# Optimization experiments

Hardware: AMD Instinct MI355X
Metric: run time of the kernel (lower is better)

The kernel has to match this reference:

```python
import jax, jax.numpy as jnp
import numpy as np

B = 128
N = 512            # num_nodes
RU = 64            # rnn_units = hidden_size // num_nodes
IN_PER_NODE = 2    # input_size // num_nodes
MEM_DIM = 16
BOT_DIM = 4
IN_SZ = IN_PER_NODE + RU      # 66, concat(input, state) per node
OUT_SZ = 4 * RU               # 256, 4 LSTM gates


def setup_inputs() -> dict:
    key = jax.random.key(0)
    ks = jax.random.split(key, 12)
    std = 1.0 / np.sqrt(N * RU)  # reset_parameters: uniform(-std, std)
    u = lambda k, shape: jax.random.uniform(k, shape, jnp.float32, -std, std)
    return {
        "inputs": jax.random.normal(ks[0], (B, N * IN_PER_NODE), jnp.float32),
        "hx": jax.random.normal(ks[1], (B, N * RU), jnp.float32),
        "cx": jax.random.normal(ks[2], (B, N * RU), jnp.float32),
        "memory": u(ks[3], (N, MEM_DIM)),
        "w1": u(ks[4], (MEM_DIM, MEM_DIM)),
        "b1": u(ks[5], (MEM_DIM,)),
        "w2": u(ks[6], (MEM_DIM, BOT_DIM)),
        "b2": u(ks[7], (BOT_DIM,)),
        "w3": u(ks[8], (BOT_DIM, IN_SZ * OUT_SZ)),
        "b3": u(ks[9], (IN_SZ * OUT_SZ,)),
        "b_out": u(ks[10], (OUT_SZ,)),
    }


def reference(inputs, hx, cx, memory, w1, b1, w2, b2, w3, b3, b_out):
    b = inputs.shape[0]
    n = memory.shape[0]
    ru = hx.shape[1] // n
    # per-node concat of input and state: [B, N, IN_SZ]
    x = inputs.reshape(b, n, -1)
    h = hx.reshape(b, n, ru)
    xs = jnp.concatenate([x, h], axis=-1)
    # hypernetwork: memory -> per-node weight matrices [N, IN_SZ, OUT_SZ]
    mem = jnp.tanh(memory @ w1 + b1)
    mem = jnp.tanh(mem @ w2 + b2)
    W = (mem @ w3 + b3).reshape(n, xs.shape[-1], -1)
    # batched per-node matmul (original repeats W over batch; same math without the repeat)
    val = jax.nn.sigmoid(jnp.einsum('bni,nio->bno', xs, W)) + b_out  # [B, N, 4*RU]
    g = val.reshape(b, n, 4, ru)
    i_t = jax.nn.sigmoid(g[:, :, 0, :].reshape(b, n * ru))
    f_t = jax.nn.sigmoid(g[:, :, 1, :].reshape(b, n * ru))
    g_t = jnp.tanh(g[:, :, 2, :].reshape(b, n * ru))
    o_t = jax.nn.sigmoid(g[:, :, 3, :].reshape(b, n * ru))
    cy = cx * f_t + i_t * g_t
    hy = o_t * jnp.tanh(cy)
    return hy, cy
```

## Files before the change

### kernel.cpp

```cpp
#include <hip/hip_runtime.h>
#include <math.h>

#define BATCH 128
#define NNODE 512
#define RU 64
#define MEM_DIM 16
#define BOT_DIM 4
#define IN_SZ 66
#define OUT_SZ 256
#define HID (NNODE*RU)
#define W3_ROW 16896
#define COL_SHORTS 104
#define NODE_W_SHORTS (256*COL_SHORTS)
#define HALF_W_SHORTS (128*COL_SHORTS)

typedef __attribute__((ext_vector_type(8))) short short8;
typedef __attribute__((ext_vector_type(4))) float float4v;

__device__ __forceinline__ unsigned short f2bf(float f) {
    unsigned int u = __float_as_uint(f);
    unsigned int r = (u + 0x7FFFu + ((u >> 16) & 1u)) >> 16;
    return (unsigned short)r;
}
__device__ __forceinline__ float fsig(float x) {
    return __builtin_amdgcn_rcpf(1.0f + __expf(-x));
}
__device__ __forceinline__ float ftanh(float x) {
    return 1.0f - 2.0f * __builtin_amdgcn_rcpf(1.0f + __expf(2.0f * x));
}

__global__ __launch_bounds__(256) void wgen_kernel(
    const float* __restrict__ memory, const float* __restrict__ w1,
    const float* __restrict__ b1,     const float* __restrict__ w2,
    const float* __restrict__ b2,     const float* __restrict__ w3,
    const float* __restrict__ b3,     unsigned short* __restrict__ W_ws)
{
    __shared__ unsigned short Wn[256][COL_SHORTS];
    const int c = threadIdx.x;
    const int n = blockIdx.x;

    float memv[MEM_DIM];
    #pragma unroll
    for (int j = 0; j < MEM_DIM; ++j) memv[j] = memory[n * MEM_DIM + j];
    float mem1[MEM_DIM];
    #pragma unroll
    for (int t = 0; t < MEM_DIM; ++t) {
        float s = b1[t];
        #pragma unroll
        for (int j = 0; j < MEM_DIM; ++j) s += memv[j] * w1[j * MEM_DIM + t];
        mem1[t] = ftanh(s);
    }
    float m[BOT_DIM];
    #pragma unroll
    for (int t = 0; t < BOT_DIM; ++t) {
        float s = b2[t];
        #pragma unroll
        for (int j = 0; j < MEM_DIM; ++j) s += mem1[j] * w2[j * BOT_DIM + t];
        m[t] = ftanh(s);
    }

    const int ct = c >> 4, q = c & 15;
    const int o = (ct & 3) * 64 + (ct >> 2) * 16 + q;
    const float* p0 = w3 + o;
    const float* pb = b3 + o;

    for (int i = 0; i < IN_SZ; ++i) {
        int j = i * OUT_SZ;
        float f = pb[j] + m[0] * p0[j] + m[1] * p0[W3_ROW + j]
                        + m[2] * p0[2 * W3_ROW + j] + m[3] * p0[3 * W3_ROW + j];
        int s = (i < 2) ? (64 + i) : (i - 2);
        Wn[c][s] = f2bf(f);
    }
    #pragma unroll
    for (int s = IN_SZ; s < COL_SHORTS; ++s) Wn[c][s] = 0;
    __syncthreads();

    unsigned short* dst = W_ws + (size_t)n * NODE_W_SHORTS + c * COL_SHORTS;
    #pragma unroll
    for (int kc = 0; kc < 13; ++kc)
        *(short8*)(dst + kc * 8) = *(const short8*)(&Wn[c][kc * 8]);
}

__global__ __launch_bounds__(256, 3) void gemm_kernel(
    const float* __restrict__ inputs, const float* __restrict__ hx,
    const float* __restrict__ cx,     const float* __restrict__ b_out,
    const unsigned short* __restrict__ W_ws, float* __restrict__ out)
{
    __shared__ unsigned short Wl[128][COL_SHORTS];
    const int tid  = threadIdx.x;
    const int n    = (int)blockIdx.x >> 1;
    const int h    = (int)blockIdx.x & 1;
    const int w    = tid >> 6;
    const int lane = tid & 63;
    const int q    = lane & 15;
    const int quad = lane >> 4;

    const unsigned short* gW = W_ws + (size_t)n * NODE_W_SHORTS + h * HALF_W_SHORTS;
    for (int t = w; t < 26; t += 4) {
        __builtin_amdgcn_global_load_lds(
            (__attribute__((address_space(1))) void*)(gW + t * 512 + lane * 8),
            (__attribute__((address_space(3))) void*)(&Wl[0][0] + t * 512),
            16, 0, 0);
    }

    short8 a[3][2];
    #pragma unroll
    for (int rt = 0; rt < 2; ++rt) {
        const int row = w * 32 + rt * 16 + q;
        const float* hrow = hx + (size_t)row * HID + n * RU + quad * 8;
        #pragma unroll
        for (int ks = 0; ks < 2; ++ks) {
            float4v f0 = *(const float4v*)(hrow + ks * 32);
            float4v f1 = *(const float4v*)(hrow + ks * 32 + 4);
            short8 t;
            t[0] = (short)f2bf(f0[0]); t[1] = (short)f2bf(f0[1]);
            t[2] = (short)f2bf(f0[2]); t[3] = (short)f2bf(f0[3]);
            t[4] = (short)f2bf(f1[0]); t[5] = (short)f2bf(f1[1]);
            t[6] = (short)f2bf(f1[2]); t[7] = (short)f2bf(f1[3]);
            a[ks][rt] = t;
        }
        short8 t2 = {0, 0, 0, 0, 0, 0, 0, 0};
        if (quad == 0) {
            const float* ip = inputs + (size_t)row * (NNODE * IN_SZ - NNODE * RU) + n * 2;
            t2[0] = (short)f2bf(ip[0]);
            t2[1] = (short)f2bf(ip[1]);
        }
        a[2][rt] = t2;
    }

    float4v acc[2][8];
    #pragma unroll
    for (int rt = 0; rt < 2; ++rt)
        #pragma unroll
        for (int ctl = 0; ctl < 8; ++ctl)
            acc[rt][ctl] = (float4v){0.f, 0.f, 0.f, 0.f};

    __syncthreads();

    #pragma unroll
    for (int ks = 0; ks < 3; ++ks) {
        #pragma unroll
        for (int ctl = 0; ctl < 8; ++ctl) {
            short8 bfrag = *(const short8*)(&Wl[ctl * 16 + q][(ks * 4 + quad) * 8]);
            acc[0][ctl] = __builtin_amdgcn_mfma_f32_16x16x32_bf16(a[ks][0], bfrag, acc[0][ctl], 0, 0, 0);
            acc[1][ctl] = __builtin_amdgcn_mfma_f32_16x16x32_bf16(a[ks][1], bfrag, acc[1][ctl], 0, 0, 0);
        }
    }

    float bo[2][4];
    #pragma unroll
    for (int rh = 0; rh < 2; ++rh)
        #pragma unroll
        for (int g = 0; g < 4; ++g)
            bo[rh][g] = b_out[g * 64 + (h * 2 + rh) * 16 + q];

    #pragma unroll
    for (int rt = 0; rt < 2; ++rt) {
        #pragma unroll
        for (int v = 0; v < 4; ++v) {
            const int b = w * 32 + rt * 16 + quad * 4 + v;
            const size_t base = (size_t)b * HID + n * RU;
            #pragma unroll
            for (int rh = 0; rh < 2; ++rh) {
                float vi = fsig(acc[rt][rh * 4 + 0][v]) + bo[rh][0];
                float vf = fsig(acc[rt][rh * 4 + 1][v]) + bo[rh][1];
                float vg = fsig(acc[rt][rh * 4 + 2][v]) + bo[rh][2];
                float vo = fsig(acc[rt][rh * 4 + 3][v]) + bo[rh][3];
                float it = fsig(vi), ft = fsig(vf);
                float gt = ftanh(vg), ot = fsig(vo);
                const size_t idx = base + (h * 2 + rh) * 16 + q;
                float cc = cx[idx] * ft + it * gt;
                out[idx] = ot * ftanh(cc);
                out[(size_t)BATCH * HID + idx] = cc;
            }
        }
    }
}

extern "C" void kernel_launch(void* const* d_in, const int* in_sizes, int n_in,
                              void* d_out, int out_size, void* d_ws, size_t ws_size,
                              hipStream_t stream) {
    const float* inputs = (const float*)d_in[0];
    const float* hx     = (const float*)d_in[1];
    const float* cx     = (const float*)d_in[2];
    const float* memory = (const float*)d_in[3];
    const float* w1     = (const float*)d_in[4];
    const float* b1     = (const float*)d_in[5];
    const float* w2     = (const float*)d_in[6];
    const float* b2     = (const float*)d_in[7];
    const float* w3     = (const float*)d_in[8];
    const float* b3     = (const float*)d_in[9];
    const float* b_out  = (const float*)d_in[10];
    float* out = (float*)d_out;

    unsigned short* W_ws = (unsigned short*)d_ws;

    wgen_kernel<<<NNODE, 256, 0, stream>>>(memory, w1, b1, w2, b2, w3, b3, W_ws);
    gemm_kernel<<<NNODE * 2, 256, 0, stream>>>(inputs, hx, cx, b_out, W_ws, out);
}
```

Measured before the change: 139.4 us.

## Tile weight-generation by output-column groups and prefetch cx before MFMA loop

The weight-generation kernel now stages a 32-column slice of w3 and b3 in shared memory once per block and reuses it across 8 nodes. Previously every node block re-read all of w3 and b3 from global memory. The output is written as coalesced 16-byte chunks. The GEMM kernel loads cx and b_out into registers before the MFMA loop so those loads overlap the matrix work, at the cost of extra registers under launch bounds of 3 blocks per SM.

```diff
diff --git a/kernel.cpp b/kernel.cpp
--- a/kernel.cpp
+++ b/kernel.cpp
@@ -13,6 +13,8 @@
 #define COL_SHORTS 104
 #define NODE_W_SHORTS (256*COL_SHORTS)
 #define HALF_W_SHORTS (128*COL_SHORTS)
+#define W3S_STRIDE 84
+#define B3S_STRIDE 72
 
 typedef __attribute__((ext_vector_type(8))) short short8;
 typedef __attribute__((ext_vector_type(4))) float float4v;
@@ -27,6 +29,10 @@
 }
 __device__ __forceinline__ float ftanh(float x) {
     return 1.0f - 2.0f * __builtin_amdgcn_rcpf(1.0f + __expf(2.0f * x));
+}
+__device__ __forceinline__ int omap(int cg, int cl) {
+    int ct = cg * 2 + (cl >> 4);
+    return (ct & 3) * 64 + ((ct >> 2) << 4) + (cl & 15);
 }
 
 __global__ __launch_bounds__(256) void wgen_kernel(
@@ -35,50 +41,92 @@
     const float* __restrict__ b2,     const float* __restrict__ w3,
     const float* __restrict__ b3,     unsigned short* __restrict__ W_ws)
 {
-    __shared__ unsigned short Wn[256][COL_SHORTS];
-    const int c = threadIdx.x;
-    const int n = blockIdx.x;
-
-    float memv[MEM_DIM];
-    #pragma unroll
-    for (int j = 0; j < MEM_DIM; ++j) memv[j] = memory[n * MEM_DIM + j];
-    float mem1[MEM_DIM];
-    #pragma unroll
-    for (int t = 0; t < MEM_DIM; ++t) {
+    __shared__ alignas(16) float w3s[4][32][W3S_STRIDE];
+    __shared__ alignas(16) float b3s[32][B3S_STRIDE];
+    __shared__ float mem1s[8][MEM_DIM];
+    __shared__ float m2s[8][BOT_DIM];
+
+    const int tid = threadIdx.x;
+    const int cg  = (int)blockIdx.x & 7;
+    const int ng  = (int)blockIdx.x >> 3;
+
+    for (int e = tid; e < 4 * 32 * 72; e += 256) {
+        int cl = e & 31;
+        int r  = e >> 5;
+        int k  = r / 72;
+        int s  = r - k * 72;
+        float v = 0.f;
+        if (s < 66) {
+            int i = (s < 64) ? s + 2 : s - 64;
+            v = w3[k * W3_ROW + i * OUT_SZ + omap(cg, cl)];
+        }
+        w3s[k][cl][s] = v;
+    }
+    for (int e = tid; e < 32 * 72; e += 256) {
+        int cl = e & 31;
+        int s  = e >> 5;
+        float v = 0.f;
+        if (s < 66) {
+            int i = (s < 64) ? s + 2 : s - 64;
+            v = b3[i * OUT_SZ + omap(cg, cl)];
+        }
+        b3s[cl][s] = v;
+    }
+
+    if (tid < 128) {
+        int nn = tid >> 4, t = tid & 15;
+        int n  = ng * 8 + nn;
         float s = b1[t];
         #pragma unroll
-        for (int j = 0; j < MEM_DIM; ++j) s += memv[j] * w1[j * MEM_DIM + t];
-        mem1[t] = ftanh(s);
-    }
-    float m[BOT_DIM];
-    #pragma unroll
-    for (int t = 0; t < BOT_DIM; ++t) {
+        for (int j = 0; j < MEM_DIM; ++j)
+            s += memory[n * MEM_DIM + j] * w1[j * MEM_DIM + t];
+        mem1s[nn][t] = ftanh(s);
+    }
+    __syncthreads();
+    if (tid < 32) {
+        int nn = tid >> 2, t = tid & 3;
         float s = b2[t];
         #pragma unroll
-        for (int j = 0; j < MEM_DIM; ++j) s += mem1[j] * w2[j * BOT_DIM + t];
-        m[t] = ftanh(s);
-    }
-
-    const int ct = c >> 4, q = c & 15;
-    const int o = (ct & 3) * 64 + (ct >> 2) * 16 + q;
-    const float* p0 = w3 + o;
-    const float* pb = b3 + o;
-
-    for (int i = 0; i < IN_SZ; ++i) {
-        int j = i * OUT_SZ;
-        float f = pb[j] + m[0] * p0[j] + m[1] * p0[W3_ROW + j]
-                        + m[2] * p0[2 * W3_ROW + j] + m[3] * p0[3 * W3_ROW + j];
-        int s = (i < 2) ? (64 + i) : (i - 2);
-        Wn[c][s] = f2bf(f);
-    }
-    #pragma unroll
-    for (int s = IN_SZ; s < COL_SHORTS; ++s) Wn[c][s] = 0;
+        for (int j = 0; j < MEM_DIM; ++j)
+            s += mem1s[nn][j] * w2[j * BOT_DIM + t];
+        m2s[nn][t] = ftanh(s);
+    }
     __syncthreads();
 
-    unsigned short* dst = W_ws + (size_t)n * NODE_W_SHORTS + c * COL_SHORTS;
-    #pragma unroll
-    for (int kc = 0; kc < 13; ++kc)
-        *(short8*)(dst + kc * 8) = *(const short8*)(&Wn[c][kc * 8]);
+    for (int p = 0; p < 4; ++p) {
+        const int n0 = ng * 8 + p * 2;
+        float ma[4], mb[4];
+        #pragma unroll
+        for (int k = 0; k < 4; ++k) { ma[k] = m2s[p * 2][k]; mb[k] = m2s[p * 2 + 1][k]; }
+
+        for (int t = tid; t < 832; t += 256) {
+            int nn2 = t >= 416;
+            int rem = nn2 ? t - 416 : t;
+            int cl  = rem / 13;
+            int sc  = rem - cl * 13;
+            short8 ov = {0, 0, 0, 0, 0, 0, 0, 0};
+            if (sc < 9) {
+                const int s0 = sc * 8;
+                float4v v0 = *(const float4v*)&b3s[cl][s0];
+                float4v v1 = *(const float4v*)&b3s[cl][s0 + 4];
+                #pragma unroll
+                for (int k = 0; k < 4; ++k) {
+                    float mk = nn2 ? mb[k] : ma[k];
+                    float4v w0 = *(const float4v*)&w3s[k][cl][s0];
+                    float4v w1v = *(const float4v*)&w3s[k][cl][s0 + 4];
+                    v0 += mk * w0;
+                    v1 += mk * w1v;
+                }
+                ov[0] = (short)f2bf(v0[0]); ov[1] = (short)f2bf(v0[1]);
+                ov[2] = (short)f2bf(v0[2]); ov[3] = (short)f2bf(v0[3]);
+                ov[4] = (short)f2bf(v1[0]); ov[5] = (short)f2bf(v1[1]);
+                ov[6] = (short)f2bf(v1[2]); ov[7] = (short)f2bf(v1[3]);
+            }
+            unsigned short* dst = W_ws + (size_t)(n0 + nn2) * NODE_W_SHORTS
+                                + cg * 3328 + cl * COL_SHORTS + sc * 8;
+            *(short8*)dst = ov;
+        }
+    }
 }
 
 __global__ __launch_bounds__(256, 3) void gemm_kernel(
@@ -121,12 +169,30 @@
         }
         short8 t2 = {0, 0, 0, 0, 0, 0, 0, 0};
         if (quad == 0) {
-            const float* ip = inputs + (size_t)row * (NNODE * IN_SZ - NNODE * RU) + n * 2;
+            const float* ip = inputs + (size_t)row * (NNODE * 2) + n * 2;
             t2[0] = (short)f2bf(ip[0]);
             t2[1] = (short)f2bf(ip[1]);
         }
         a[2][rt] = t2;
     }
+
+    float cxr[2][4][2];
+    #pragma unroll
+    for (int rt = 0; rt < 2; ++rt)
+        #pragma unroll
+        for (int v = 0; v < 4; ++v) {
+            const int b = w * 32 + rt * 16 + quad * 4 + v;
+            #pragma unroll
+            for (int rh = 0; rh < 2; ++rh)
+                cxr[rt][v][rh] = cx[(size_t)b * HID + n * RU + (h * 2 + rh) * 16 + q];
+        }
+
+    float bo[2][4];
+    #pragma unroll
+    for (int rh = 0; rh < 2; ++rh)
+        #pragma unroll
+        for (int g = 0; g < 4; ++g)
+            bo[rh][g] = b_out[g * 64 + (h * 2 + rh) * 16 + q];
 
     float4v acc[2][8];
     #pragma unroll
@@ -146,13 +212,6 @@
             acc[1][ctl] = __builtin_amdgcn_mfma_f32_16x16x32_bf16(a[ks][1], bfrag, acc[1][ctl], 0, 0, 0);
         }
     }
-
-    float bo[2][4];
-    #pragma unroll
-    for (int rh = 0; rh < 2; ++rh)
-        #pragma unroll
-        for (int g = 0; g < 4; ++g)
-            bo[rh][g] = b_out[g * 64 + (h * 2 + rh) * 16 + q];
 
     #pragma unroll
     for (int rt = 0; rt < 2; ++rt) {
@@ -169,7 +228,7 @@
                 float it = fsig(vi), ft = fsig(vf);
                 float gt = ftanh(vg), ot = fsig(vo);
                 const size_t idx = base + (h * 2 + rh) * 16 + q;
-                float cc = cx[idx] * ft + it * gt;
+                float cc = cxr[rt][v][rh] * ft + it * gt;
                 out[idx] = ot * ftanh(cc);
                 out[(size_t)BATCH * HID + idx] = cc;
             }
```

Result: no change. 136.7 us (-1.9%).

## Pre-swizzle weights into MFMA fragment order and split GEMM into quarter-node blocks

Applied to the files above, without the earlier changes.

The weight generator now writes bf16 weights directly in per-lane MFMA B-fragment order, and each block handles two nodes so every w3/b3 load is reused twice. The GEMM kernel drops the LDS staging and the barrier and reads fragments straight from global memory with 16-byte loads. Each block now covers a quarter of a node's output columns, giving 2048 blocks and fewer accumulators, with occupancy raised to 4. cx is prefetched before the MFMA loop. The trade-offs are redundant hx loads across four blocks per node and extra wgen grid work.

```diff
diff --git a/kernel.cpp b/kernel.cpp
--- a/kernel.cpp
+++ b/kernel.cpp
@@ -10,9 +10,8 @@
 #define OUT_SZ 256
 #define HID (NNODE*RU)
 #define W3_ROW 16896
-#define COL_SHORTS 104
-#define NODE_W_SHORTS (256*COL_SHORTS)
-#define HALF_W_SHORTS (128*COL_SHORTS)
+#define NODE_WS 24576
+#define HALF_WS 12288
 
 typedef __attribute__((ext_vector_type(8))) short short8;
 typedef __attribute__((ext_vector_type(4))) float float4v;
@@ -35,73 +34,94 @@
     const float* __restrict__ b2,     const float* __restrict__ w3,
     const float* __restrict__ b3,     unsigned short* __restrict__ W_ws)
 {
-    __shared__ unsigned short Wn[256][COL_SHORTS];
-    const int c = threadIdx.x;
-    const int n = blockIdx.x;
-
-    float memv[MEM_DIM];
-    #pragma unroll
-    for (int j = 0; j < MEM_DIM; ++j) memv[j] = memory[n * MEM_DIM + j];
-    float mem1[MEM_DIM];
-    #pragma unroll
-    for (int t = 0; t < MEM_DIM; ++t) {
+    __shared__ float mem1s[2][MEM_DIM];
+    __shared__ float m2s[2][BOT_DIM];
+
+    const int tid   = threadIdx.x;
+    const unsigned bid = blockIdx.x;
+    const int npair = bid >> 2;
+    const int h     = (bid >> 1) & 1;
+    const int fg    = bid & 1;
+    const int n0    = npair * 2;
+
+    if (tid < 32) {
+        int nn = tid >> 4, t = tid & 15;
         float s = b1[t];
         #pragma unroll
-        for (int j = 0; j < MEM_DIM; ++j) s += memv[j] * w1[j * MEM_DIM + t];
-        mem1[t] = ftanh(s);
-    }
-    float m[BOT_DIM];
-    #pragma unroll
-    for (int t = 0; t < BOT_DIM; ++t) {
+        for (int j = 0; j < MEM_DIM; ++j)
+            s += memory[(n0 + nn) * MEM_DIM + j] * w1[j * MEM_DIM + t];
+        mem1s[nn][t] = ftanh(s);
+    }
+    __syncthreads();
+    if (tid < 8) {
+        int nn = tid >> 2, t = tid & 3;
         float s = b2[t];
         #pragma unroll
-        for (int j = 0; j < MEM_DIM; ++j) s += mem1[j] * w2[j * BOT_DIM + t];
-        m[t] = ftanh(s);
-    }
-
-    const int ct = c >> 4, q = c & 15;
-    const int o = (ct & 3) * 64 + (ct >> 2) * 16 + q;
-    const float* p0 = w3 + o;
-    const float* pb = b3 + o;
-
-    for (int i = 0; i < IN_SZ; ++i) {
-        int j = i * OUT_SZ;
-        float f = pb[j] + m[0] * p0[j] + m[1] * p0[W3_ROW + j]
-                        + m[2] * p0[2 * W3_ROW + j] + m[3] * p0[3 * W3_ROW + j];
-        int s = (i < 2) ? (64 + i) : (i - 2);
-        Wn[c][s] = f2bf(f);
-    }
-    #pragma unroll
-    for (int s = IN_SZ; s < COL_SHORTS; ++s) Wn[c][s] = 0;
+        for (int j = 0; j < MEM_DIM; ++j)
+            s += mem1s[nn][j] * w2[j * BOT_DIM + t];
+        m2s[nn][t] = ftanh(s);
+    }
     __syncthreads();
 
-    unsigned short* dst = W_ws + (size_t)n * NODE_W_SHORTS + c * COL_SHORTS;
-    #pragma unroll
-    for (int kc = 0; kc < 13; ++kc)
-        *(short8*)(dst + kc * 8) = *(const short8*)(&Wn[c][kc * 8]);
-}
-
-__global__ __launch_bounds__(256, 3) void gemm_kernel(
+    float ma[4], mb[4];
+    #pragma unroll
+    for (int k = 0; k < 4; ++k) { ma[k] = m2s[0][k]; mb[k] = m2s[1][k]; }
+
+    unsigned short* dst0 = W_ws + (size_t)n0 * NODE_WS + h * HALF_WS;
+    unsigned short* dst1 = dst0 + NODE_WS;
+
+    #pragma unroll 2
+    for (int it = 0; it < 6; ++it) {
+        const int cid = it * 256 + tid;
+        const int fl  = fg * 12 + (cid >> 6);
+        const int l   = cid & 63;
+        const int ctl = fl / 3;
+        const int ks  = fl - ctl * 3;
+        const int q = l & 15, quad = l >> 4;
+        const int ct = h * 8 + ctl;
+        const int o  = (ct & 3) * 64 + ((ct >> 2) << 4) + q;
+
+        short8 va, vb;
+        #pragma unroll
+        for (int j = 0; j < 8; ++j) {
+            const int s = ks * 32 + quad * 8 + j;
+            float r0 = 0.f, r1 = 0.f;
+            if (s < IN_SZ) {
+                const int i = (s < 64) ? s + 2 : s - 64;
+                const int base = i * OUT_SZ + o;
+                float bb = b3[base];
+                float x0 = w3[base];
+                float x1 = w3[W3_ROW + base];
+                float x2 = w3[2 * W3_ROW + base];
+                float x3 = w3[3 * W3_ROW + base];
+                r0 = bb + ma[0] * x0 + ma[1] * x1 + ma[2] * x2 + ma[3] * x3;
+                r1 = bb + mb[0] * x0 + mb[1] * x1 + mb[2] * x2 + mb[3] * x3;
+            }
+            va[j] = (short)f2bf(r0);
+            vb[j] = (short)f2bf(r1);
+        }
+        const int off = fl * 512 + l * 8;
+        *(short8*)(dst0 + off) = va;
+        *(short8*)(dst1 + off) = vb;
+    }
+}
+
+__global__ __launch_bounds__(256, 4) void gemm_kernel(
     const float* __restrict__ inputs, const float* __restrict__ hx,
     const float* __restrict__ cx,     const float* __restrict__ b_out,
     const unsigned short* __restrict__ W_ws, float* __restrict__ out)
 {
-    __shared__ unsigned short Wl[128][COL_SHORTS];
     const int tid  = threadIdx.x;
-    const int n    = (int)blockIdx.x >> 1;
-    const int h    = (int)blockIdx.x & 1;
+    const unsigned bid = blockIdx.x;
+    const int n    = bid >> 2;
+    const int qh   = bid & 3;
     const int w    = tid >> 6;
     const int lane = tid & 63;
     const int q    = lane & 15;
     const int quad = lane >> 4;
 
-    const unsigned short* gW = W_ws + (size_t)n * NODE_W_SHORTS + h * HALF_W_SHORTS;
-    for (int t = w; t < 26; t += 4) {
-        __builtin_amdgcn_global_load_lds(
-            (__attribute__((address_space(1))) void*)(gW + t * 512 + lane * 8),
-            (__attribute__((address_space(3))) void*)(&Wl[0][0] + t * 512),
-            16, 0, 0);
-    }
+    const unsigned short* Wb = W_ws + (size_t)n * NODE_WS + (qh >> 1) * HALF_WS
+                             + (qh & 1) * 4 * 3 * 512;
 
     short8 a[3][2];
     #pragma unroll
@@ -121,58 +141,59 @@
         }
         short8 t2 = {0, 0, 0, 0, 0, 0, 0, 0};
         if (quad == 0) {
-            const float* ip = inputs + (size_t)row * (NNODE * IN_SZ - NNODE * RU) + n * 2;
+            const float* ip = inputs + (size_t)row * (NNODE * 2) + n * 2;
             t2[0] = (short)f2bf(ip[0]);
             t2[1] = (short)f2bf(ip[1]);
         }
         a[2][rt] = t2;
     }
 
-    float4v acc[2][8];
+    const int r = qh * 16 + q;
+    float bo[4];
+    #pragma unroll
+    for (int g = 0; g < 4; ++g) bo[g] = b_out[g * 64 + r];
+
+    float cxr[2][4];
     #pragma unroll
     for (int rt = 0; rt < 2; ++rt)
-        #pragma unroll
-        for (int ctl = 0; ctl < 8; ++ctl)
-            acc[rt][ctl] = (float4v){0.f, 0.f, 0.f, 0.f};
-
-    __syncthreads();
-
-    #pragma unroll
-    for (int ks = 0; ks < 3; ++ks) {
-        #pragma unroll
-        for (int ctl = 0; ctl < 8; ++ctl) {
-            short8 bfrag = *(const short8*)(&Wl[ctl * 16 + q][(ks * 4 + quad) * 8]);
-            acc[0][ctl] = __builtin_amdgcn_mfma_f32_16x16x32_bf16(a[ks][0], bfrag, acc[0][ctl], 0, 0, 0);
-            acc[1][ctl] = __builtin_amdgcn_mfma_f32_16x16x32_bf16(a[ks][1], bfrag, acc[1][ctl], 0, 0, 0);
-        }
-    }
-
-    float bo[2][4];
-    #pragma unroll
-    for (int rh = 0; rh < 2; ++rh)
-        #pragma unroll
-        for (int g = 0; g < 4; ++g)
-            bo[rh][g] = b_out[g * 64 + (h * 2 + rh) * 16 + q];
-
-    #pragma unroll
-    for (int rt = 0; rt < 2; ++rt) {
         #pragma unroll
         for (int v = 0; v < 4; ++v) {
             const int b = w * 32 + rt * 16 + quad * 4 + v;
-            const size_t base = (size_t)b * HID + n * RU;
-            #pragma unroll
-            for (int rh = 0; rh < 2; ++rh) {
-                float vi = fsig(acc[rt][rh * 4 + 0][v]) + bo[rh][0];
-                float vf = fsig(acc[rt][rh * 4 + 1][v]) + bo[rh][1];
-                float vg = fsig(acc[rt][rh * 4 + 2][v]) + bo[rh][2];
-                float vo = fsig(acc[rt][rh * 4 + 3][v]) + bo[rh][3];
-                float it = fsig(vi), ft = fsig(vf);
-                float gt = ftanh(vg), ot = fsig(vo);
-                const size_t idx = base + (h * 2 + rh) * 16 + q;
-                float cc = cx[idx] * ft + it * gt;
-                out[idx] = ot * ftanh(cc);
-                out[(size_t)BATCH * HID + idx] = cc;
-            }
+            cxr[rt][v] = cx[(size_t)b * HID + n * RU + r];
+        }
+
+    float4v acc[2][4];
+    #pragma unroll
+    for (int rt = 0; rt < 2; ++rt)
+        #pragma unroll
+        for (int g = 0; g < 4; ++g)
+            acc[rt][g] = (float4v){0.f, 0.f, 0.f, 0.f};
+
+    #pragma unroll
+    for (int ks = 0; ks < 3; ++ks) {
+        #pragma unroll
+        for (int g = 0; g < 4; ++g) {
+            short8 bf = *(const short8*)(Wb + (g * 3 + ks) * 512 + lane * 8);
+            acc[0][g] = __builtin_amdgcn_mfma_f32_16x16x32_bf16(a[ks][0], bf, acc[0][g], 0, 0, 0);
+            acc[1][g] = __builtin_amdgcn_mfma_f32_16x16x32_bf16(a[ks][1], bf, acc[1][g], 0, 0, 0);
+        }
+    }
+
+    #pragma unroll
+    for (int rt = 0; rt < 2; ++rt) {
+        #pragma unroll
+        for (int v = 0; v < 4; ++v) {
+            const int b = w * 32 + rt * 16 + quad * 4 + v;
+            const size_t idx = (size_t)b * HID + n * RU + r;
+            float vi = fsig(acc[rt][0][v]) + bo[0];
+            float vf = fsig(acc[rt][1][v]) + bo[1];
+            float vg = fsig(acc[rt][2][v]) + bo[2];
+            float vo = fsig(acc[rt][3][v]) + bo[3];
+            float it = fsig(vi), ft = fsig(vf);
+            float gt = ftanh(vg), ot = fsig(vo);
+            float cc = cxr[rt][v] * ft + it * gt;
+            out[idx] = ot * ftanh(cc);
+            out[(size_t)BATCH * HID + idx] = cc;
         }
     }
 }
@@ -195,6 +216,6 @@
 
     unsigned short* W_ws = (unsigned short*)d_ws;
 
-    wgen_kernel<<<NNODE, 256, 0, stream>>>(memory, w1, b1, w2, b2, w3, b3, W_ws);
-    gemm_kernel<<<NNODE * 2, 256, 0, stream>>>(inputs, hx, cx, b_out, W_ws, out);
-}
+    wgen_kernel<<<256 * 4, 256, 0, stream>>>(memory, w1, b1, w2, b2, w3, b3, W_ws);
+    gemm_kernel<<<NNODE * 4, 256, 0, stream>>>(inputs, hx, cx, b_out, W_ws, out);
+}
```

After: 144.5 us. 1.04x slower.

## Factor hypernetwork weights through rank-5 basis instead of materializing per-node weights

Applied to the files above, without the earlier changes.

Per-node weight matrices W_n = sum_k m_k*w3_k + b3 are no longer built. The kernel instead precomputes five shared bf16 basis matrices (w3 rows and b3) in MFMA fragment layout and scales the activations by each node's coefficient m_k, accumulating five GEMMs. This removes the 512 per-node weight tiles (about 27 MB of workspace written and read back) in exchange for five times the MFMA work and extra bf16 conversions. The basis is small and is read straight from global/L2 without LDS staging. Each node now uses one 512-thread block, and cx is loaded before the matmul.

```diff
diff --git a/kernel.cpp b/kernel.cpp
--- a/kernel.cpp
+++ b/kernel.cpp
@@ -10,9 +10,7 @@
 #define OUT_SZ 256
 #define HID (NNODE*RU)
 #define W3_ROW 16896
-#define COL_SHORTS 104
-#define NODE_W_SHORTS (256*COL_SHORTS)
-#define HALF_W_SHORTS (128*COL_SHORTS)
+#define W5_BYTES (240*512*2)
 
 typedef __attribute__((ext_vector_type(8))) short short8;
 typedef __attribute__((ext_vector_type(4))) float float4v;
@@ -29,150 +27,176 @@
     return 1.0f - 2.0f * __builtin_amdgcn_rcpf(1.0f + __expf(2.0f * x));
 }
 
-__global__ __launch_bounds__(256) void wgen_kernel(
+__global__ __launch_bounds__(256) void prep_kernel(
     const float* __restrict__ memory, const float* __restrict__ w1,
     const float* __restrict__ b1,     const float* __restrict__ w2,
     const float* __restrict__ b2,     const float* __restrict__ w3,
-    const float* __restrict__ b3,     unsigned short* __restrict__ W_ws)
+    const float* __restrict__ b3,     unsigned short* __restrict__ W5,
+    float* __restrict__ m2_ws)
 {
-    __shared__ unsigned short Wn[256][COL_SHORTS];
-    const int c = threadIdx.x;
-    const int n = blockIdx.x;
-
-    float memv[MEM_DIM];
-    #pragma unroll
-    for (int j = 0; j < MEM_DIM; ++j) memv[j] = memory[n * MEM_DIM + j];
-    float mem1[MEM_DIM];
-    #pragma unroll
-    for (int t = 0; t < MEM_DIM; ++t) {
-        float s = b1[t];
-        #pragma unroll
-        for (int j = 0; j < MEM_DIM; ++j) s += memv[j] * w1[j * MEM_DIM + t];
-        mem1[t] = ftanh(s);
-    }
-    float m[BOT_DIM];
-    #pragma unroll
-    for (int t = 0; t < BOT_DIM; ++t) {
-        float s = b2[t];
-        #pragma unroll
-        for (int j = 0; j < MEM_DIM; ++j) s += mem1[j] * w2[j * BOT_DIM + t];
-        m[t] = ftanh(s);
-    }
-
-    const int ct = c >> 4, q = c & 15;
-    const int o = (ct & 3) * 64 + (ct >> 2) * 16 + q;
-    const float* p0 = w3 + o;
-    const float* pb = b3 + o;
-
-    for (int i = 0; i < IN_SZ; ++i) {
-        int j = i * OUT_SZ;
-        float f = pb[j] + m[0] * p0[j] + m[1] * p0[W3_ROW + j]
-                        + m[2] * p0[2 * W3_ROW + j] + m[3] * p0[3 * W3_ROW + j];
-        int s = (i < 2) ? (64 + i) : (i - 2);
-        Wn[c][s] = f2bf(f);
-    }
-    #pragma unroll
-    for (int s = IN_SZ; s < COL_SHORTS; ++s) Wn[c][s] = 0;
-    __syncthreads();
-
-    unsigned short* dst = W_ws + (size_t)n * NODE_W_SHORTS + c * COL_SHORTS;
-    #pragma unroll
-    for (int kc = 0; kc < 13; ++kc)
-        *(short8*)(dst + kc * 8) = *(const short8*)(&Wn[c][kc * 8]);
-}
-
-__global__ __launch_bounds__(256, 3) void gemm_kernel(
+    const int tid = threadIdx.x;
+    const int bid = blockIdx.x;
+    if (bid < 60) {
+        const int c    = bid * 256 + tid;
+        const int lane = c & 63;
+        const int f    = c >> 6;
+        const int ks   = f % 3;
+        const int t2   = f / 3;
+        const int ct   = t2 & 15;
+        const int k    = t2 >> 4;
+        const int q = lane & 15, quad = lane >> 4;
+        const int o = (ct & 3) * 64 + (ct >> 2) * 16 + q;
+        const float* src = (k < 4) ? (w3 + k * W3_ROW) : b3;
+        short8 v;
+        #pragma unroll
+        for (int j = 0; j < 8; ++j) {
+            const int s = ks * 32 + quad * 8 + j;
+            float x = 0.f;
+            if (s < IN_SZ) {
+                const int i = (s < 64) ? s + 2 : s - 64;
+                x = src[i * OUT_SZ + o];
+            }
+            v[j] = (short)f2bf(x);
+        }
+        *(short8*)(W5 + f * 512 + lane * 8) = v;
+    } else {
+        const int n = (bid - 60) * 256 + tid;
+        if (n < NNODE) {
+            float memv[MEM_DIM];
+            #pragma unroll
+            for (int j = 0; j < MEM_DIM; ++j) memv[j] = memory[n * MEM_DIM + j];
+            float mem1[MEM_DIM];
+            #pragma unroll
+            for (int t = 0; t < MEM_DIM; ++t) {
+                float s = b1[t];
+                #pragma unroll
+                for (int j = 0; j < MEM_DIM; ++j) s += memv[j] * w1[j * MEM_DIM + t];
+                mem1[t] = ftanh(s);
+            }
+            #pragma unroll
+            for (int t = 0; t < BOT_DIM; ++t) {
+                float s = b2[t];
+                #pragma unroll
+                for (int j = 0; j < MEM_DIM; ++j) s += mem1[j] * w2[j * BOT_DIM + t];
+                m2_ws[n * 4 + t] = ftanh(s);
+            }
+        }
+    }
+}
+
+__global__ __launch_bounds__(512, 2) void fused_kernel(
     const float* __restrict__ inputs, const float* __restrict__ hx,
     const float* __restrict__ cx,     const float* __restrict__ b_out,
-    const unsigned short* __restrict__ W_ws, float* __restrict__ out)
+    const unsigned short* __restrict__ W5, const float* __restrict__ m2_ws,
+    float* __restrict__ out)
 {
-    __shared__ unsigned short Wl[128][COL_SHORTS];
     const int tid  = threadIdx.x;
-    const int n    = (int)blockIdx.x >> 1;
-    const int h    = (int)blockIdx.x & 1;
+    const int n    = blockIdx.x;
     const int w    = tid >> 6;
     const int lane = tid & 63;
+    const int rh   = w >> 2;
+    const int qh   = w & 3;
     const int q    = lane & 15;
     const int quad = lane >> 4;
 
-    const unsigned short* gW = W_ws + (size_t)n * NODE_W_SHORTS + h * HALF_W_SHORTS;
-    for (int t = w; t < 26; t += 4) {
-        __builtin_amdgcn_global_load_lds(
-            (__attribute__((address_space(1))) void*)(gW + t * 512 + lane * 8),
-            (__attribute__((address_space(3))) void*)(&Wl[0][0] + t * 512),
-            16, 0, 0);
-    }
-
-    short8 a[3][2];
-    #pragma unroll
-    for (int rt = 0; rt < 2; ++rt) {
-        const int row = w * 32 + rt * 16 + q;
+    float coef[5];
+    #pragma unroll
+    for (int k = 0; k < 4; ++k) coef[k] = m2_ws[n * 4 + k];
+    coef[4] = 1.0f;
+
+    float4v xa[4][4];
+    float xin[4][2];
+    #pragma unroll
+    for (int rt = 0; rt < 4; ++rt) {
+        const int row = rh * 64 + rt * 16 + q;
         const float* hrow = hx + (size_t)row * HID + n * RU + quad * 8;
-        #pragma unroll
-        for (int ks = 0; ks < 2; ++ks) {
-            float4v f0 = *(const float4v*)(hrow + ks * 32);
-            float4v f1 = *(const float4v*)(hrow + ks * 32 + 4);
-            short8 t;
-            t[0] = (short)f2bf(f0[0]); t[1] = (short)f2bf(f0[1]);
-            t[2] = (short)f2bf(f0[2]); t[3] = (short)f2bf(f0[3]);
-            t[4] = (short)f2bf(f1[0]); t[5] = (short)f2bf(f1[1]);
-            t[6] = (short)f2bf(f1[2]); t[7] = (short)f2bf(f1[3]);
-            a[ks][rt] = t;
-        }
-        short8 t2 = {0, 0, 0, 0, 0, 0, 0, 0};
+        xa[rt][0] = *(const float4v*)(hrow);
+        xa[rt][1] = *(const float4v*)(hrow + 4);
+        xa[rt][2] = *(const float4v*)(hrow + 32);
+        xa[rt][3] = *(const float4v*)(hrow + 36);
         if (quad == 0) {
-            const float* ip = inputs + (size_t)row * (NNODE * IN_SZ - NNODE * RU) + n * 2;
-            t2[0] = (short)f2bf(ip[0]);
-            t2[1] = (short)f2bf(ip[1]);
-        }
-        a[2][rt] = t2;
-    }
-
-    float4v acc[2][8];
-    #pragma unroll
-    for (int rt = 0; rt < 2; ++rt)
-        #pragma unroll
-        for (int ctl = 0; ctl < 8; ++ctl)
-            acc[rt][ctl] = (float4v){0.f, 0.f, 0.f, 0.f};
-
-    __syncthreads();
-
-    #pragma unroll
-    for (int ks = 0; ks < 3; ++ks) {
-        #pragma unroll
-        for (int ctl = 0; ctl < 8; ++ctl) {
-            short8 bfrag = *(const short8*)(&Wl[ctl * 16 + q][(ks * 4 + quad) * 8]);
-            acc[0][ctl] = __builtin_amdgcn_mfma_f32_16x16x32_bf16(a[ks][0], bfrag, acc[0][ctl], 0, 0, 0);
-            acc[1][ctl] = __builtin_amdgcn_mfma_f32_16x16x32_bf16(a[ks][1], bfrag, acc[1][ctl], 0, 0, 0);
-        }
-    }
-
-    float bo[2][4];
-    #pragma unroll
-    for (int rh = 0; rh < 2; ++rh)
+            const float* ip = inputs + (size_t)row * (NNODE * 2) + n * 2;
+            xin[rt][0] = ip[0];
+            xin[rt][1] = ip[1];
+        } else {
+            xin[rt][0] = 0.f;
+            xin[rt][1] = 0.f;
+        }
+    }
+
+    const int r = qh * 16 + q;
+    float bo[4];
+    #pragma unroll
+    for (int g = 0; g < 4; ++g) bo[g] = b_out[g * 64 + r];
+    float cxr[4][4];
+    #pragma unroll
+    for (int rt = 0; rt < 4; ++rt)
+        #pragma unroll
+        for (int v = 0; v < 4; ++v) {
+            const int b = rh * 64 + rt * 16 + quad * 4 + v;
+            cxr[rt][v] = cx[(size_t)b * HID + n * RU + r];
+        }
+
+    float4v acc[4][4];
+    #pragma unroll
+    for (int rt = 0; rt < 4; ++rt)
         #pragma unroll
         for (int g = 0; g < 4; ++g)
-            bo[rh][g] = b_out[g * 64 + (h * 2 + rh) * 16 + q];
-
-    #pragma unroll
-    for (int rt = 0; rt < 2; ++rt) {
+            acc[rt][g] = (float4v){0.f, 0.f, 0.f, 0.f};
+
+    #pragma unroll
+    for (int k = 0; k < 5; ++k) {
+        const float cf = coef[k];
+        short8 af[3][4];
+        #pragma unroll
+        for (int rt = 0; rt < 4; ++rt) {
+            #pragma unroll
+            for (int ksh = 0; ksh < 2; ++ksh) {
+                float4v lo = xa[rt][ksh * 2];
+                float4v hi = xa[rt][ksh * 2 + 1];
+                if (k < 4) { lo *= cf; hi *= cf; }
+                short8 t;
+                t[0] = (short)f2bf(lo[0]); t[1] = (short)f2bf(lo[1]);
+                t[2] = (short)f2bf(lo[2]); t[3] = (short)f2bf(lo[3]);
+                t[4] = (short)f2bf(hi[0]); t[5] = (short)f2bf(hi[1]);
+                t[6] = (short)f2bf(hi[2]); t[7] = (short)f2bf(hi[3]);
+                af[ksh][rt] = t;
+            }
+            float a0 = xin[rt][0], a1 = xin[rt][1];
+            if (k < 4) { a0 *= cf; a1 *= cf; }
+            short8 t2 = {0, 0, 0, 0, 0, 0, 0, 0};
+            t2[0] = (short)f2bf(a0);
+            t2[1] = (short)f2bf(a1);
+            af[2][rt] = t2;
+        }
+        #pragma unroll
+        for (int ks = 0; ks < 3; ++ks)
+            #pragma unroll
+            for (int g = 0; g < 4; ++g) {
+                const short8 bf = *(const short8*)(
+                    W5 + (size_t)((k * 16 + qh * 4 + g) * 3 + ks) * 512 + lane * 8);
+                #pragma unroll
+                for (int rt = 0; rt < 4; ++rt)
+                    acc[rt][g] = __builtin_amdgcn_mfma_f32_16x16x32_bf16(
+                        af[ks][rt], bf, acc[rt][g], 0, 0, 0);
+            }
+    }
+
+    #pragma unroll
+    for (int rt = 0; rt < 4; ++rt) {
         #pragma unroll
         for (int v = 0; v < 4; ++v) {
-            const int b = w * 32 + rt * 16 + quad * 4 + v;
-            const size_t base = (size_t)b * HID + n * RU;
-            #pragma unroll
-            for (int rh = 0; rh < 2; ++rh) {
-                float vi = fsig(acc[rt][rh * 4 + 0][v]) + bo[rh][0];
-                float vf = fsig(acc[rt][rh * 4 + 1][v]) + bo[rh][1];
-                float vg = fsig(acc[rt][rh * 4 + 2][v]) + bo[rh][2];
-                float vo = fsig(acc[rt][rh * 4 + 3][v]) + bo[rh][3];
-                float it = fsig(vi), ft = fsig(vf);
-                float gt = ftanh(vg), ot = fsig(vo);
-                const size_t idx = base + (h * 2 + rh) * 16 + q;
-                float cc = cx[idx] * ft + it * gt;
-                out[idx] = ot * ftanh(cc);
-                out[(size_t)BATCH * HID + idx] = cc;
-            }
+            const int b = rh * 64 + rt * 16 + quad * 4 + v;
+            const size_t idx = (size_t)b * HID + n * RU + r;
+            float vi = fsig(acc[rt][0][v]) + bo[0];
+            float vf = fsig(acc[rt][1][v]) + bo[1];
+            float vg = fsig(acc[rt][2][v]) + bo[2];
+            float vo = fsig(acc[rt][3][v]) + bo[3];
+            float it = fsig(vi), ft = fsig(vf);
+            float gt = ftanh(vg), ot = fsig(vo);
+            float cc = cxr[rt][v] * ft + it * gt;
+            out[idx] = ot * ftanh(cc);
+            out[(size_t)BATCH * HID + idx] = cc;
         }
     }
 }
@@ -193,8 +217,9 @@
     const float* b_out  = (const float*)d_in[10];
     float* out = (float*)d_out;
 
-    unsigned short* W_ws = (unsigned short*)d_ws;
-
-    wgen_kernel<<<NNODE, 256, 0, stream>>>(memory, w1, b1, w2, b2, w3, b3, W_ws);
-    gemm_kernel<<<NNODE * 2, 256, 0, stream>>>(inputs, hx, cx, b_out, W_ws, out);
-}
+    unsigned short* W5 = (unsigned short*)d_ws;
+    float* m2_ws = (float*)((char*)d_ws + W5_BYTES);
+
+    prep_kernel<<<62, 256, 0, stream>>>(memory, w1, b1, w2, b2, w3, b3, W5, m2_ws);
+    fused_kernel<<<NNODE, 512, 0, stream>>>(inputs, hx, cx, b_out, W5, m2_ws, out);
+}
```

Result: no change. 138.1 us (-1.0%).
